# Performance work log

Hardware: AMD Instinct MI355X
Metric: run time of the kernel (lower is better)

Reference implementation:

```python
import jax, jax.numpy as jnp
import numpy as np

NUM_HEADS = 16

def setup_inputs() -> dict:
    key = jax.random.key(0)
    ks = jax.random.split(key, 7)
    query_dim, kv_dim, out_dim = 1024, 768, 1024
    N, Lq, Lkv = 4, 2048, 2048
    s_q = 1.0 / np.sqrt(query_dim)
    s_kv = 1.0 / np.sqrt(kv_dim)
    return {
        "query": jax.random.normal(ks[0], (N, Lq, query_dim), dtype=jnp.float32),
        "kv": jax.random.normal(ks[1], (N, Lkv, kv_dim), dtype=jnp.float32),
        # Linear weights stored as (in_dim, out_dim) for x @ W
        "Wq": jax.random.uniform(ks[2], (query_dim, query_dim), jnp.float32, -s_q, s_q),
        "Wk": jax.random.uniform(ks[3], (kv_dim, query_dim), jnp.float32, -s_kv, s_kv),
        "Wv": jax.random.uniform(ks[4], (kv_dim, query_dim), jnp.float32, -s_kv, s_kv),
        "Wo": jax.random.uniform(ks[5], (query_dim, out_dim), jnp.float32, -s_q, s_q),
        "bo": jax.random.uniform(ks[6], (out_dim,), jnp.float32, -s_q, s_q),
    }

def reference(query, kv, Wq, Wk, Wv, Wo, bo):
    N, Lq, qd = query.shape
    Lkv = kv.shape[1]
    H = NUM_HEADS
    hd = qd // H
    scale = hd ** -0.5
    # projections -> (N, H, L, hd)
    q = (query @ Wq).reshape(N, Lq, H, hd).transpose(0, 2, 1, 3)
    k = (kv @ Wk).reshape(N, Lkv, H, hd).transpose(0, 2, 1, 3)
    v = (kv @ Wv).reshape(N, Lkv, H, hd).transpose(0, 2, 1, 3)
    # fp32 attention: (N, H, Lq, Lkv)
    attn = jnp.einsum('bhqd,bhkd->bhqk', q.astype(jnp.float32) * scale, k.astype(jnp.float32))
    attn = jax.nn.softmax(attn, axis=-1)
    out = jnp.einsum('bhqk,bhkd->bhqd', attn, v.astype(jnp.float32))
    out = out.transpose(0, 2, 1, 3).reshape(N, Lq, qd)
    return out @ Wo + bo
```

## Files before the change

kernel.cpp:

```cpp
#include <hip/hip_runtime.h>

typedef __attribute__((ext_vector_type(4))) float f32x4;
typedef __attribute__((ext_vector_type(8))) __bf16 bf16x8;
typedef __attribute__((ext_vector_type(8))) unsigned short us8;

__device__ __forceinline__ unsigned short f2bf(float f) {
    unsigned u = __builtin_bit_cast(unsigned, f);
    u += 0x7fffu + ((u >> 16) & 1u);
    return (unsigned short)(u >> 16);
}

__device__ __forceinline__ float exp2v(float x) {
    float r;
    asm("v_exp_f32 %0, %1" : "=v"(r) : "v"(x));
    return r;
}

__device__ __forceinline__ f32x4 mfma16(bf16x8 a, bf16x8 b, f32x4 c) {
    return __builtin_amdgcn_mfma_f32_16x16x32_bf16(a, b, c, 0, 0, 0);
}

__device__ __forceinline__ void gload16(const void* g, void* l) {
    __builtin_amdgcn_global_load_lds(
        (const __attribute__((address_space(1))) unsigned int*)g,
        (__attribute__((address_space(3))) unsigned int*)l, 16, 0, 0);
}

__global__ __launch_bounds__(256) void conv2_bf16(const float* __restrict__ a,
                                                  unsigned short* __restrict__ oa,
                                                  int na8,
                                                  const float* __restrict__ b,
                                                  unsigned short* __restrict__ ob,
                                                  int nb8) {
    int i = blockIdx.x * 256 + threadIdx.x;
    const float* in;
    unsigned short* out;
    if (i < na8) {
        in = a; out = oa;
    } else {
        i -= na8;
        if (i >= nb8) return;
        in = b; out = ob;
    }
    const float4* p = (const float4*)in + (size_t)i * 2;
    float4 x = p[0], y = p[1];
    us8 o;
    o[0] = f2bf(x.x); o[1] = f2bf(x.y); o[2] = f2bf(x.z); o[3] = f2bf(x.w);
    o[4] = f2bf(y.x); o[5] = f2bf(y.y); o[6] = f2bf(y.z); o[7] = f2bf(y.w);
    *((us8*)out + i) = o;
}

__global__ __launch_bounds__(256) void wtrans_all(const float* __restrict__ Wq,
                                                  const float* __restrict__ Wk,
                                                  const float* __restrict__ Wv,
                                                  const float* __restrict__ Wo,
                                                  unsigned short* __restrict__ WqT,
                                                  unsigned short* __restrict__ WkT,
                                                  unsigned short* __restrict__ WvT,
                                                  unsigned short* __restrict__ WoT,
                                                  float qscale) {
    __shared__ float t[32][33];
    int y = blockIdx.y;
    const float* in; unsigned short* out; int R; float scale = 1.0f;
    if (y < 32)      { in = Wq; out = WqT; R = 1024; scale = qscale; }
    else if (y < 56) { in = Wk; out = WkT; R = 768;  y -= 32; }
    else if (y < 80) { in = Wv; out = WvT; R = 768;  y -= 56; }
    else             { in = Wo; out = WoT; R = 1024; y -= 80; }
    int tx = threadIdx.x, ty = threadIdx.y;
    int r0 = y * 32, c0 = blockIdx.x * 32;
#pragma unroll
    for (int k = 0; k < 4; ++k)
        t[ty + k * 8][tx] = in[(size_t)(r0 + ty + k * 8) * 1024 + c0 + tx];
    __syncthreads();
#pragma unroll
    for (int k = 0; k < 4; ++k)
        out[(size_t)(c0 + ty + k * 8) * R + r0 + tx] = f2bf(t[tx][ty + k * 8] * scale);
}

__global__ __launch_bounds__(256, 4) void proj_qkv(const unsigned short* __restrict__ qbf,
                                                   const unsigned short* __restrict__ kvbf,
                                                   const unsigned short* __restrict__ WqT,
                                                   const unsigned short* __restrict__ WkT,
                                                   const unsigned short* __restrict__ WvT,
                                                   unsigned short* __restrict__ Qh,
                                                   unsigned short* __restrict__ Kh,
                                                   unsigned short* __restrict__ VTh) {
    __shared__ __align__(16) unsigned short SL[2][8192];
    const int id = blockIdx.x;
    const int xcd = id & 7, j = id >> 3;
    const int my = xcd * 8 + (j & 7);
    const int rest = j >> 3;
    const int op = rest >> 3;
    const int nx = rest & 7;
    const int m0 = my * 128, n0 = nx * 128;
    const unsigned short* A = (op == 0) ? qbf : kvbf;
    const unsigned short* B = (op == 0) ? WqT : (op == 1 ? WkT : WvT);
    const int KD = (op == 0) ? 1024 : 768;
    const int NT = KD >> 5;

    const int tid = threadIdx.x;
    const int w = tid >> 6, l = tid & 63;
    const int lr = l & 15, lg = l >> 4;
    const int wm = (w >> 1) * 64, wn = (w & 1) * 64;

    f32x4 acc[4][4] = {};

    int ci0 = w * 64 + l;
    int r0 = ci0 >> 2, c0 = (ci0 & 3) ^ (r0 & 3);
    int ci1 = 256 + ci0;
    int r1 = ci1 >> 2, c1 = (ci1 & 3) ^ (r1 & 3);

    const unsigned short* Ag0 = A + (size_t)(m0 + r0) * KD + c0 * 8;
    const unsigned short* Ag1 = A + (size_t)(m0 + r1) * KD + c1 * 8;
    const unsigned short* Bg0 = B + (size_t)(n0 + r0) * KD + c0 * 8;
    const unsigned short* Bg1 = B + (size_t)(n0 + r1) * KD + c1 * 8;

#define STG(buf, k0)                                                  \
    do {                                                              \
        gload16(Ag0 + (k0), &SL[buf][w * 512]);                       \
        gload16(Ag1 + (k0), &SL[buf][2048 + w * 512]);                \
        gload16(Bg0 + (k0), &SL[buf][4096 + w * 512]);                \
        gload16(Bg1 + (k0), &SL[buf][4096 + 2048 + w * 512]);         \
    } while (0)

    STG(0, 0);
    int buf = 0;
    for (int kt = 0; kt < NT; ++kt) {
        if (kt + 1 < NT) {
            STG(buf ^ 1, (kt + 1) * 32);
            asm volatile("s_waitcnt vmcnt(4)" ::: "memory");
        } else {
            asm volatile("s_waitcnt vmcnt(0)" ::: "memory");
        }
        __builtin_amdgcn_s_barrier();
        const unsigned short* Alc = &SL[buf][0];
        const unsigned short* Blc = &SL[buf][4096];
        bf16x8 af[4], bfr[4];
#pragma unroll
        for (int t = 0; t < 4; ++t) {
            int ar = wm + t * 16 + lr;
            af[t] = *(const bf16x8*)&Alc[ar * 32 + ((lg ^ (ar & 3)) * 8)];
            int br = wn + t * 16 + lr;
            bfr[t] = *(const bf16x8*)&Blc[br * 32 + ((lg ^ (br & 3)) * 8)];
        }
#pragma unroll
        for (int i = 0; i < 4; ++i)
#pragma unroll
            for (int jj = 0; jj < 4; ++jj)
                acc[i][jj] = mfma16(af[i], bfr[jj], acc[i][jj]);
        __builtin_amdgcn_s_barrier();
        buf ^= 1;
    }
#undef STG

    if (op != 2) {
        unsigned short* Cout = (op == 0) ? Qh : Kh;
#pragma unroll
        for (int i = 0; i < 4; ++i)
#pragma unroll
            for (int jj = 0; jj < 4; ++jj)
#pragma unroll
                for (int r = 0; r < 4; ++r) {
                    int m = m0 + wm + i * 16 + lg * 4 + r;
                    int n = n0 + wn + jj * 16 + lr;
                    int b = m >> 11, ql = m & 2047, h = n >> 6, d = n & 63;
                    Cout[(((size_t)(b * 16 + h) * 2048 + ql) << 6) + d] = f2bf(acc[i][jj][r]);
                }
    } else {
        const int b = m0 >> 11;
        const int mloc = m0 & 2047;
        const int h0 = n0 >> 6;
#pragma unroll
        for (int hp = 0; hp < 2; ++hp) {
            unsigned short* VTb = VTh + (size_t)(b * 16 + h0 + hp) * (64 * 2048);
#pragma unroll
            for (int dh = 0; dh < 2; ++dh) {
                __syncthreads();
                if ((w & 1) == hp) {
#pragma unroll
                    for (int jj = 0; jj < 2; ++jj) {
                        int jc = dh * 2 + jj;
                        int dl = jj * 16 + lr;
#pragma unroll
                        for (int i = 0; i < 4; ++i)
#pragma unroll
                            for (int r = 0; r < 4; ++r) {
                                int kvl = wm + i * 16 + lg * 4 + r;
                                int pl = (kvl & 0x60) | (((kvl >> 2) & 3) << 3) |
                                         (((kvl >> 4) & 1) << 2) | (kvl & 3);
                                SL[0][dl * 136 + pl] = f2bf(acc[i][jc][r]);
                            }
                    }
                }
                __syncthreads();
#pragma unroll
                for (int cc = 0; cc < 2; ++cc) {
                    int idx = cc * 256 + tid;
                    int row = idx >> 4, col = (idx & 15) * 8;
                    *(us8*)&VTb[(size_t)(dh * 32 + row) * 2048 + mloc + col] =
                        *(const us8*)&SL[0][row * 136 + col];
                }
            }
        }
    }
}

__global__ __launch_bounds__(256, 4) void gemm_o(const unsigned short* __restrict__ A,
                                                 const unsigned short* __restrict__ B,
                                                 float* __restrict__ Cout,
                                                 const float* __restrict__ bias) {
    constexpr int KD = 1024;
    __shared__ __align__(16) unsigned short SL[2][8192];
    const int id = blockIdx.x;
    const int xcd = id & 7, j = id >> 3;
    const int m0 = (xcd * 8 + (j & 7)) * 128;
    const int n0 = (j >> 3) * 128;
    const int tid = threadIdx.x;
    const int w = tid >> 6, l = tid & 63;
    const int lr = l & 15, lg = l >> 4;
    const int wm = (w >> 1) * 64, wn = (w & 1) * 64;

    f32x4 acc[4][4] = {};

    int ci0 = w * 64 + l;
    int r0 = ci0 >> 2, c0 = (ci0 & 3) ^ (r0 & 3);
    int ci1 = 256 + ci0;
    int r1 = ci1 >> 2, c1 = (ci1 & 3) ^ (r1 & 3);

    const unsigned short* Ag0 = A + (size_t)(m0 + r0) * KD + c0 * 8;
    const unsigned short* Ag1 = A + (size_t)(m0 + r1) * KD + c1 * 8;
    const unsigned short* Bg0 = B + (size_t)(n0 + r0) * KD + c0 * 8;
    const unsigned short* Bg1 = B + (size_t)(n0 + r1) * KD + c1 * 8;

#define STG(buf, k0)                                                  \
    do {                                                              \
        gload16(Ag0 + (k0), &SL[buf][w * 512]);                       \
        gload16(Ag1 + (k0), &SL[buf][2048 + w * 512]);                \
        gload16(Bg0 + (k0), &SL[buf][4096 + w * 512]);                \
        gload16(Bg1 + (k0), &SL[buf][4096 + 2048 + w * 512]);         \
    } while (0)

    constexpr int NT = KD >> 5;
    STG(0, 0);
    int buf = 0;
    for (int kt = 0; kt < NT; ++kt) {
        if (kt + 1 < NT) {
            STG(buf ^ 1, (kt + 1) * 32);
            asm volatile("s_waitcnt vmcnt(4)" ::: "memory");
        } else {
            asm volatile("s_waitcnt vmcnt(0)" ::: "memory");
        }
        __builtin_amdgcn_s_barrier();
        const unsigned short* Alc = &SL[buf][0];
        const unsigned short* Blc = &SL[buf][4096];
        bf16x8 af[4], bfr[4];
#pragma unroll
        for (int t = 0; t < 4; ++t) {
            int ar = wm + t * 16 + lr;
            af[t] = *(const bf16x8*)&Alc[ar * 32 + ((lg ^ (ar & 3)) * 8)];
            int br = wn + t * 16 + lr;
            bfr[t] = *(const bf16x8*)&Blc[br * 32 + ((lg ^ (br & 3)) * 8)];
        }
#pragma unroll
        for (int i = 0; i < 4; ++i)
#pragma unroll
            for (int jj = 0; jj < 4; ++jj)
                acc[i][jj] = mfma16(af[i], bfr[jj], acc[i][jj]);
        __builtin_amdgcn_s_barrier();
        buf ^= 1;
    }
#undef STG

#pragma unroll
    for (int i = 0; i < 4; ++i)
#pragma unroll
        for (int jj = 0; jj < 4; ++jj)
#pragma unroll
            for (int r = 0; r < 4; ++r) {
                int m = m0 + wm + i * 16 + lg * 4 + r;
                int n = n0 + wn + jj * 16 + lr;
                Cout[(size_t)m * 1024 + n] = acc[i][jj][r] + bias[n];
            }
}

__global__ __launch_bounds__(256, 2) void attn_fwd(const unsigned short* __restrict__ Q,
                                                   const unsigned short* __restrict__ K,
                                                   const unsigned short* __restrict__ VT,
                                                   unsigned short* __restrict__ O) {
    __shared__ __align__(16) unsigned short Kl[2][64 * 64];
    __shared__ __align__(16) unsigned short Vl[2][64 * 64];
    const int id = blockIdx.x;
    const int sw = (id & 7) * 64 + (id >> 3);
    const int qt = sw & 7, bh = sw >> 3;
    const int tid = threadIdx.x;
    const int w = tid >> 6, l = tid & 63;
    const int lr = l & 15, lg = l >> 4;
    const size_t hbase = (size_t)bh * (2048 * 64);
    const size_t vbase = (size_t)bh * (64 * 2048);
    const int qbase = qt * 256 + w * 64;

    bf16x8 qf[4][2];
#pragma unroll
    for (int rt = 0; rt < 4; ++rt) {
        const unsigned short* qp = Q + hbase + (size_t)(qbase + rt * 16 + lr) * 64;
        qf[rt][0] = *(const bf16x8*)(qp + lg * 8);
        qf[rt][1] = *(const bf16x8*)(qp + 32 + lg * 8);
    }

    f32x4 oacc[4][4] = {};
    f32x4 lacc[4] = {};
    const f32x4 FZERO = {};

    bf16x8 ONES;
#pragma unroll
    for (int e = 0; e < 8; ++e) ONES[e] = (__bf16)1.0f;

    const int cA = tid, cB = 256 + tid;
    const int krA = cA >> 3, kcA = (cA & 7) ^ (krA & 7);
    const int krB = cB >> 3, kcB = (cB & 7) ^ (krB & 7);
    const unsigned short* Kg0 = K + hbase + (size_t)krA * 64 + kcA * 8;
    const unsigned short* Kg1 = K + hbase + (size_t)krB * 64 + kcB * 8;
    const unsigned short* Vg0 = VT + vbase + (size_t)krA * 2048 + kcA * 8;
    const unsigned short* Vg1 = VT + vbase + (size_t)krB * 2048 + kcB * 8;

#define STAGE_KV(dst, kv0)                                                    \
    do {                                                                      \
        gload16(Kg0 + (size_t)(kv0) * 64, &Kl[dst][w * 512]);                 \
        gload16(Kg1 + (size_t)(kv0) * 64, &Kl[dst][2048 + w * 512]);          \
        gload16(Vg0 + (kv0), &Vl[dst][w * 512]);                              \
        gload16(Vg1 + (kv0), &Vl[dst][2048 + w * 512]);                       \
    } while (0)

    const int koff0 = lr * 64 + ((lg ^ (lr & 7)) * 8);
    const int koff1 = lr * 64 + (((4 + lg) ^ (lr & 7)) * 8);

    STAGE_KV(0, 0);
    int cur = 0;

    for (int t = 0; t < 32; ++t) {
        if (t < 31) {
            STAGE_KV(cur ^ 1, (t + 1) * 64);
            asm volatile("s_waitcnt vmcnt(4)" ::: "memory");
        } else {
            asm volatile("s_waitcnt vmcnt(0)" ::: "memory");
        }
        __builtin_amdgcn_s_barrier();
        const unsigned short* Kc = Kl[cur];
        const unsigned short* Vc = Vl[cur];

        f32x4 s[4][4];
        __builtin_amdgcn_s_setprio(1);
#pragma unroll
        for (int nt = 0; nt < 4; ++nt) {
            bf16x8 kf0 = *(const bf16x8*)&Kc[koff0 + nt * 1024];
            bf16x8 kf1 = *(const bf16x8*)&Kc[koff1 + nt * 1024];
#pragma unroll
            for (int rt = 0; rt < 4; ++rt) {
                s[rt][nt] = mfma16(kf0, qf[rt][0], FZERO);
                s[rt][nt] = mfma16(kf1, qf[rt][1], s[rt][nt]);
            }
        }
        __builtin_amdgcn_s_setprio(0);

        bf16x8 pa0[4], pa1[4];
#pragma unroll
        for (int rt = 0; rt < 4; ++rt) {
#pragma unroll
            for (int nt = 0; nt < 4; ++nt)
#pragma unroll
                for (int r = 0; r < 4; ++r)
                    s[rt][nt][r] = exp2v(s[rt][nt][r]);
#pragma unroll
            for (int e = 0; e < 4; ++e) {
                pa0[rt][e] = (__bf16)s[rt][0][e];
                pa0[rt][4 + e] = (__bf16)s[rt][1][e];
                pa1[rt][e] = (__bf16)s[rt][2][e];
                pa1[rt][4 + e] = (__bf16)s[rt][3][e];
            }
        }

        __builtin_amdgcn_s_setprio(1);
#pragma unroll
        for (int rt = 0; rt < 4; ++rt) {
            lacc[rt] = mfma16(pa0[rt], ONES, lacc[rt]);
            lacc[rt] = mfma16(pa1[rt], ONES, lacc[rt]);
        }
#pragma unroll
        for (int nt = 0; nt < 4; ++nt) {
            bf16x8 vb0 = *(const bf16x8*)&Vc[koff0 + nt * 1024];
            bf16x8 vb1 = *(const bf16x8*)&Vc[koff1 + nt * 1024];
#pragma unroll
            for (int rt = 0; rt < 4; ++rt) {
                oacc[rt][nt] = mfma16(pa0[rt], vb0, oacc[rt][nt]);
                oacc[rt][nt] = mfma16(pa1[rt], vb1, oacc[rt][nt]);
            }
        }
        __builtin_amdgcn_s_setprio(0);
        __builtin_amdgcn_s_barrier();
        cur ^= 1;
    }
#undef STAGE_KV

    const int b = bh >> 4, h = bh & 15;
#pragma unroll
    for (int rt = 0; rt < 4; ++rt)
#pragma unroll
        for (int r = 0; r < 4; ++r) {
            float inv = 1.0f / lacc[rt][r];
            int q = qbase + rt * 16 + lg * 4 + r;
            size_t rowbase = ((size_t)(b * 2048 + q)) * 1024 + h * 64;
#pragma unroll
            for (int nt = 0; nt < 4; ++nt)
                O[rowbase + nt * 16 + lr] = f2bf(oacc[rt][nt][r] * inv);
        }
}

extern "C" void kernel_launch(void* const* d_in, const int* in_sizes, int n_in,
                              void* d_out, int out_size, void* d_ws, size_t ws_size,
                              hipStream_t stream) {
    (void)in_sizes; (void)n_in; (void)out_size; (void)ws_size;
    const float* query = (const float*)d_in[0];
    const float* kv    = (const float*)d_in[1];
    const float* Wq    = (const float*)d_in[2];
    const float* Wk    = (const float*)d_in[3];
    const float* Wv    = (const float*)d_in[4];
    const float* Wo    = (const float*)d_in[5];
    const float* bo    = (const float*)d_in[6];
    float* out = (float*)d_out;

    char* ws = (char*)d_ws;
    unsigned short* qbf  = (unsigned short*)(ws + 0);
    unsigned short* kvbf = (unsigned short*)(ws + 16777216);
    unsigned short* WkT  = (unsigned short*)(ws + 29360128);
    unsigned short* WvT  = (unsigned short*)(ws + 30932992);
    unsigned short* WqT  = (unsigned short*)(ws + 32505856);
    unsigned short* WoT  = (unsigned short*)(ws + 34603008);
    unsigned short* Qh   = (unsigned short*)(ws + 36700160);
    unsigned short* Kh   = (unsigned short*)(ws + 53477376);
    unsigned short* VTh  = (unsigned short*)(ws + 70254592);
    unsigned short* Ob   = (unsigned short*)(ws + 16777216);

    const float QSCALE = 0.18033688011112042f;

    conv2_bf16<<<7168, 256, 0, stream>>>(query, qbf, 1048576, kv, kvbf, 786432);
    wtrans_all<<<dim3(32, 112), dim3(32, 8), 0, stream>>>(Wq, Wk, Wv, Wo,
                                                          WqT, WkT, WvT, WoT, QSCALE);

    proj_qkv<<<1536, 256, 0, stream>>>(qbf, kvbf, WqT, WkT, WvT, Qh, Kh, VTh);
    attn_fwd<<<512, 256, 0, stream>>>(Qh, Kh, VTh, Ob);
    gemm_o<<<512, 256, 0, stream>>>(Ob, WoT, out, bo);
}
```

Baseline: 161.8 us.

## Switch attention to 32x32 MFMA with smaller q tiles and fuse prep kernels

Attention now uses 32x32x16 bf16 MFMA with 32 query rows per wave, halving the per-block query tile, doubling the grid, and raising occupancy to 3 blocks per CU. The V-transpose permutation in the projection kernel is changed to match the new MFMA operand layout. The bf16 conversion and weight transpose kernels are merged into one launch to save a launch. The intent is fewer MFMA instructions per FLOP and better latency hiding, but K/V tiles are reloaded by twice as many blocks.

```diff
diff --git a/kernel.cpp b/kernel.cpp
--- a/kernel.cpp
+++ b/kernel.cpp
@@ -1,6 +1,7 @@
 #include <hip/hip_runtime.h>
 
 typedef __attribute__((ext_vector_type(4))) float f32x4;
+typedef __attribute__((ext_vector_type(16))) float f32x16;
 typedef __attribute__((ext_vector_type(8))) __bf16 bf16x8;
 typedef __attribute__((ext_vector_type(8))) unsigned short us8;
 
@@ -20,61 +21,68 @@
     return __builtin_amdgcn_mfma_f32_16x16x32_bf16(a, b, c, 0, 0, 0);
 }
 
+__device__ __forceinline__ f32x16 mfma32(bf16x8 a, bf16x8 b, f32x16 c) {
+    return __builtin_amdgcn_mfma_f32_32x32x16_bf16(a, b, c, 0, 0, 0);
+}
+
 __device__ __forceinline__ void gload16(const void* g, void* l) {
     __builtin_amdgcn_global_load_lds(
         (const __attribute__((address_space(1))) unsigned int*)g,
         (__attribute__((address_space(3))) unsigned int*)l, 16, 0, 0);
 }
 
-__global__ __launch_bounds__(256) void conv2_bf16(const float* __restrict__ a,
-                                                  unsigned short* __restrict__ oa,
-                                                  int na8,
-                                                  const float* __restrict__ b,
-                                                  unsigned short* __restrict__ ob,
-                                                  int nb8) {
-    int i = blockIdx.x * 256 + threadIdx.x;
-    const float* in;
-    unsigned short* out;
-    if (i < na8) {
-        in = a; out = oa;
+__global__ __launch_bounds__(256) void prep(const float* __restrict__ query,
+                                            const float* __restrict__ kv,
+                                            const float* __restrict__ Wq,
+                                            const float* __restrict__ Wk,
+                                            const float* __restrict__ Wv,
+                                            const float* __restrict__ Wo,
+                                            unsigned short* __restrict__ qbf,
+                                            unsigned short* __restrict__ kvbf,
+                                            unsigned short* __restrict__ WqT,
+                                            unsigned short* __restrict__ WkT,
+                                            unsigned short* __restrict__ WvT,
+                                            unsigned short* __restrict__ WoT,
+                                            float qscale) {
+    __shared__ float t[32][33];
+    const int bid = blockIdx.x;
+    const int tid = threadIdx.x;
+    if (bid < 7168) {
+        int i = bid * 256 + tid;
+        const float* in;
+        unsigned short* out;
+        if (i < 1048576) {
+            in = query; out = qbf;
+        } else {
+            i -= 1048576;
+            if (i >= 786432) return;
+            in = kv; out = kvbf;
+        }
+        const float4* p = (const float4*)in + (size_t)i * 2;
+        float4 x = p[0], y = p[1];
+        us8 o;
+        o[0] = f2bf(x.x); o[1] = f2bf(x.y); o[2] = f2bf(x.z); o[3] = f2bf(x.w);
+        o[4] = f2bf(y.x); o[5] = f2bf(y.y); o[6] = f2bf(y.z); o[7] = f2bf(y.w);
+        *((us8*)out + i) = o;
     } else {
-        i -= na8;
-        if (i >= nb8) return;
-        in = b; out = ob;
-    }
-    const float4* p = (const float4*)in + (size_t)i * 2;
-    float4 x = p[0], y = p[1];
-    us8 o;
-    o[0] = f2bf(x.x); o[1] = f2bf(x.y); o[2] = f2bf(x.z); o[3] = f2bf(x.w);
-    o[4] = f2bf(y.x); o[5] = f2bf(y.y); o[6] = f2bf(y.z); o[7] = f2bf(y.w);
-    *((us8*)out + i) = o;
-}
-
-__global__ __launch_bounds__(256) void wtrans_all(const float* __restrict__ Wq,
-                                                  const float* __restrict__ Wk,
-                                                  const float* __restrict__ Wv,
-                                                  const float* __restrict__ Wo,
-                                                  unsigned short* __restrict__ WqT,
-                                                  unsigned short* __restrict__ WkT,
-                                                  unsigned short* __restrict__ WvT,
-                                                  unsigned short* __restrict__ WoT,
-                                                  float qscale) {
-    __shared__ float t[32][33];
-    int y = blockIdx.y;
-    const float* in; unsigned short* out; int R; float scale = 1.0f;
-    if (y < 32)      { in = Wq; out = WqT; R = 1024; scale = qscale; }
-    else if (y < 56) { in = Wk; out = WkT; R = 768;  y -= 32; }
-    else if (y < 80) { in = Wv; out = WvT; R = 768;  y -= 56; }
-    else             { in = Wo; out = WoT; R = 1024; y -= 80; }
-    int tx = threadIdx.x, ty = threadIdx.y;
-    int r0 = y * 32, c0 = blockIdx.x * 32;
-#pragma unroll
-    for (int k = 0; k < 4; ++k)
-        t[ty + k * 8][tx] = in[(size_t)(r0 + ty + k * 8) * 1024 + c0 + tx];
-    __syncthreads();
-#pragma unroll
-    for (int k = 0; k < 4; ++k)
-        out[(size_t)(c0 + ty + k * 8) * R + r0 + tx] = f2bf(t[tx][ty + k * 8] * scale);
+        int b2 = bid - 7168;
+        int c0 = (b2 & 31) * 32;
+        int y = b2 >> 5;
+        const float* in; unsigned short* out; int R; float scale = 1.0f;
+        if (y < 32)      { in = Wq; out = WqT; R = 1024; scale = qscale; }
+        else if (y < 56) { in = Wk; out = WkT; R = 768;  y -= 32; }
+        else if (y < 80) { in = Wv; out = WvT; R = 768;  y -= 56; }
+        else             { in = Wo; out = WoT; R = 1024; y -= 80; }
+        int tx = tid & 31, ty = tid >> 5;
+        int r0 = y * 32;
+#pragma unroll
+        for (int k = 0; k < 4; ++k)
+            t[ty + k * 8][tx] = in[(size_t)(r0 + ty + k * 8) * 1024 + c0 + tx];
+        __syncthreads();
+#pragma unroll
+        for (int k = 0; k < 4; ++k)
+            out[(size_t)(c0 + ty + k * 8) * R + r0 + tx] = f2bf(t[tx][ty + k * 8] * scale);
+    }
 }
 
 __global__ __launch_bounds__(256, 4) void proj_qkv(const unsigned short* __restrict__ qbf,
@@ -186,8 +194,9 @@
 #pragma unroll
                             for (int r = 0; r < 4; ++r) {
                                 int kvl = wm + i * 16 + lg * 4 + r;
-                                int pl = (kvl & 0x60) | (((kvl >> 2) & 3) << 3) |
-                                         (((kvl >> 4) & 1) << 2) | (kvl & 3);
+                                int pl = (kvl & 0x60) | (((kvl >> 4) & 1) << 4) |
+                                         (((kvl >> 2) & 1) << 3) |
+                                         (((kvl >> 3) & 1) << 2) | (kvl & 3);
                                 SL[0][dl * 136 + pl] = f2bf(acc[i][jc][r]);
                             }
                     }
@@ -283,33 +292,31 @@
             }
 }
 
-__global__ __launch_bounds__(256, 2) void attn_fwd(const unsigned short* __restrict__ Q,
+__global__ __launch_bounds__(256, 3) void attn_fwd(const unsigned short* __restrict__ Q,
                                                    const unsigned short* __restrict__ K,
                                                    const unsigned short* __restrict__ VT,
                                                    unsigned short* __restrict__ O) {
     __shared__ __align__(16) unsigned short Kl[2][64 * 64];
     __shared__ __align__(16) unsigned short Vl[2][64 * 64];
     const int id = blockIdx.x;
-    const int sw = (id & 7) * 64 + (id >> 3);
-    const int qt = sw & 7, bh = sw >> 3;
+    const int sw = (id & 7) * 128 + (id >> 3);
+    const int qt = sw & 15, bh = sw >> 4;
     const int tid = threadIdx.x;
     const int w = tid >> 6, l = tid & 63;
-    const int lr = l & 15, lg = l >> 4;
+    const int lq = l & 31, hi = l >> 5;
     const size_t hbase = (size_t)bh * (2048 * 64);
     const size_t vbase = (size_t)bh * (64 * 2048);
-    const int qbase = qt * 256 + w * 64;
-
-    bf16x8 qf[4][2];
-#pragma unroll
-    for (int rt = 0; rt < 4; ++rt) {
-        const unsigned short* qp = Q + hbase + (size_t)(qbase + rt * 16 + lr) * 64;
-        qf[rt][0] = *(const bf16x8*)(qp + lg * 8);
-        qf[rt][1] = *(const bf16x8*)(qp + 32 + lg * 8);
-    }
-
-    f32x4 oacc[4][4] = {};
-    f32x4 lacc[4] = {};
-    const f32x4 FZERO = {};
+    const int qbase = qt * 128 + w * 32;
+
+    bf16x8 qf[4];
+    {
+        const unsigned short* qp = Q + hbase + (size_t)(qbase + lq) * 64 + hi * 8;
+#pragma unroll
+        for (int ks = 0; ks < 4; ++ks) qf[ks] = *(const bf16x8*)(qp + ks * 16);
+    }
+
+    f32x16 oacc0 = {}, oacc1 = {}, lacc = {};
+    const f32x16 FZ16 = {};
 
     bf16x8 ONES;
 #pragma unroll
@@ -331,8 +338,7 @@
         gload16(Vg1 + (kv0), &Vl[dst][2048 + w * 512]);                       \
     } while (0)
 
-    const int koff0 = lr * 64 + ((lg ^ (lr & 7)) * 8);
-    const int koff1 = lr * 64 + (((4 + lg) ^ (lr & 7)) * 8);
+    const int swz = lq & 7;
 
     STAGE_KV(0, 0);
     int cur = 0;
@@ -348,52 +354,46 @@
         const unsigned short* Kc = Kl[cur];
         const unsigned short* Vc = Vl[cur];
 
-        f32x4 s[4][4];
+        f32x16 s0 = FZ16, s1 = FZ16;
         __builtin_amdgcn_s_setprio(1);
 #pragma unroll
-        for (int nt = 0; nt < 4; ++nt) {
-            bf16x8 kf0 = *(const bf16x8*)&Kc[koff0 + nt * 1024];
-            bf16x8 kf1 = *(const bf16x8*)&Kc[koff1 + nt * 1024];
-#pragma unroll
-            for (int rt = 0; rt < 4; ++rt) {
-                s[rt][nt] = mfma16(kf0, qf[rt][0], FZERO);
-                s[rt][nt] = mfma16(kf1, qf[rt][1], s[rt][nt]);
-            }
+        for (int ks = 0; ks < 4; ++ks) {
+            int c = ((2 * ks + hi) ^ swz) * 8;
+            bf16x8 kf0 = *(const bf16x8*)&Kc[lq * 64 + c];
+            bf16x8 kf1 = *(const bf16x8*)&Kc[(32 + lq) * 64 + c];
+            s0 = mfma32(kf0, qf[ks], s0);
+            s1 = mfma32(kf1, qf[ks], s1);
         }
         __builtin_amdgcn_s_setprio(0);
 
-        bf16x8 pa0[4], pa1[4];
-#pragma unroll
-        for (int rt = 0; rt < 4; ++rt) {
-#pragma unroll
-            for (int nt = 0; nt < 4; ++nt)
-#pragma unroll
-                for (int r = 0; r < 4; ++r)
-                    s[rt][nt][r] = exp2v(s[rt][nt][r]);
-#pragma unroll
-            for (int e = 0; e < 4; ++e) {
-                pa0[rt][e] = (__bf16)s[rt][0][e];
-                pa0[rt][4 + e] = (__bf16)s[rt][1][e];
-                pa1[rt][e] = (__bf16)s[rt][2][e];
-                pa1[rt][4 + e] = (__bf16)s[rt][3][e];
-            }
+#pragma unroll
+        for (int e = 0; e < 16; ++e) {
+            s0[e] = exp2v(s0[e]);
+            s1[e] = exp2v(s1[e]);
+        }
+        bf16x8 pa00, pa01, pa10, pa11;
+#pragma unroll
+        for (int e = 0; e < 8; ++e) {
+            pa00[e] = (__bf16)s0[e];
+            pa01[e] = (__bf16)s0[8 + e];
+            pa10[e] = (__bf16)s1[e];
+            pa11[e] = (__bf16)s1[8 + e];
         }
 
         __builtin_amdgcn_s_setprio(1);
-#pragma unroll
-        for (int rt = 0; rt < 4; ++rt) {
-            lacc[rt] = mfma16(pa0[rt], ONES, lacc[rt]);
-            lacc[rt] = mfma16(pa1[rt], ONES, lacc[rt]);
-        }
-#pragma unroll
-        for (int nt = 0; nt < 4; ++nt) {
-            bf16x8 vb0 = *(const bf16x8*)&Vc[koff0 + nt * 1024];
-            bf16x8 vb1 = *(const bf16x8*)&Vc[koff1 + nt * 1024];
-#pragma unroll
-            for (int rt = 0; rt < 4; ++rt) {
-                oacc[rt][nt] = mfma16(pa0[rt], vb0, oacc[rt][nt]);
-                oacc[rt][nt] = mfma16(pa1[rt], vb1, oacc[rt][nt]);
-            }
+        lacc = mfma32(pa00, ONES, lacc);
+        lacc = mfma32(pa01, ONES, lacc);
+        lacc = mfma32(pa10, ONES, lacc);
+        lacc = mfma32(pa11, ONES, lacc);
+
+#pragma unroll
+        for (int ks = 0; ks < 4; ++ks) {
+            int c = ((2 * ks + hi) ^ swz) * 8;
+            bf16x8 vb0 = *(const bf16x8*)&Vc[lq * 64 + c];
+            bf16x8 vb1 = *(const bf16x8*)&Vc[(32 + lq) * 64 + c];
+            bf16x8 pa = (ks == 0) ? pa00 : (ks == 1) ? pa01 : (ks == 2) ? pa10 : pa11;
+            oacc0 = mfma32(pa, vb0, oacc0);
+            oacc1 = mfma32(pa, vb1, oacc1);
         }
         __builtin_amdgcn_s_setprio(0);
         __builtin_amdgcn_s_barrier();
@@ -403,16 +403,13 @@
 
     const int b = bh >> 4, h = bh & 15;
 #pragma unroll
-    for (int rt = 0; rt < 4; ++rt)
-#pragma unroll
-        for (int r = 0; r < 4; ++r) {
-            float inv = 1.0f / lacc[rt][r];
-            int q = qbase + rt * 16 + lg * 4 + r;
-            size_t rowbase = ((size_t)(b * 2048 + q)) * 1024 + h * 64;
-#pragma unroll
-            for (int nt = 0; nt < 4; ++nt)
-                O[rowbase + nt * 16 + lr] = f2bf(oacc[rt][nt][r] * inv);
-        }
+    for (int reg = 0; reg < 16; ++reg) {
+        float inv = 1.0f / lacc[reg];
+        int q = qbase + (reg & 3) + 8 * (reg >> 2) + 4 * hi;
+        size_t rowbase = ((size_t)(b * 2048 + q)) * 1024 + h * 64;
+        O[rowbase + lq] = f2bf(oacc0[reg] * inv);
+        O[rowbase + 32 + lq] = f2bf(oacc1[reg] * inv);
+    }
 }
 
 extern "C" void kernel_launch(void* const* d_in, const int* in_sizes, int n_in,
@@ -442,11 +439,9 @@
 
     const float QSCALE = 0.18033688011112042f;
 
-    conv2_bf16<<<7168, 256, 0, stream>>>(query, qbf, 1048576, kv, kvbf, 786432);
-    wtrans_all<<<dim3(32, 112), dim3(32, 8), 0, stream>>>(Wq, Wk, Wv, Wo,
-                                                          WqT, WkT, WvT, WoT, QSCALE);
-
+    prep<<<10752, 256, 0, stream>>>(query, kv, Wq, Wk, Wv, Wo,
+                                    qbf, kvbf, WqT, WkT, WvT, WoT, QSCALE);
     proj_qkv<<<1536, 256, 0, stream>>>(qbf, kvbf, WqT, WkT, WvT, Qh, Kh, VTh);
-    attn_fwd<<<512, 256, 0, stream>>>(Qh, Kh, VTh, Ob);
+    attn_fwd<<<1024, 256, 0, stream>>>(Qh, Kh, VTh, Ob);
     gemm_o<<<512, 256, 0, stream>>>(Ob, WoT, out, bo);
 }
```

Result: slower. 173.4 us (+7.2%).
